# Optimization experiments

Measured on AMD Instinct MI355X. Metric: run time of the kernel, lower is better.

The kernel has to match this reference:

```python
import jax, jax.numpy as jnp
import numpy as np

OMEGA = 30.0
B = 65536
NUM_FREQ = 8  # int(base_dim / in_features) = 32 / 4


def _siren_w(k, out_dim, in_dim, first=False):
    bound = (1.0 / in_dim) if first else (np.sqrt(6.0 / in_dim) / OMEGA)
    return jax.random.uniform(k, (out_dim, in_dim), jnp.float32, -bound, bound)


def _lin_w(k, out_dim, in_dim):
    bound = np.sqrt(1.0 / in_dim)
    return jax.random.uniform(k, (out_dim, in_dim), jnp.float32, -bound, bound)


def setup_inputs() -> dict:
    key = jax.random.key(0)
    ks = jax.random.split(key, 16)
    E = 7
    d = {}
    d['x'] = jax.random.uniform(ks[0], (B, 4), jnp.float32, -1.0, 1.0)
    # encoder: pos_dim=64 -> sine1(128) -> sine2(256) -> resblock(256, bottleneck 128)
    d['enc_s1_w'] = _siren_w(ks[1], 128, 64, first=True); d['enc_s1_b'] = jnp.zeros((128,), jnp.float32)
    d['enc_s2_w'] = _siren_w(ks[2], 256, 128); d['enc_s2_b'] = jnp.zeros((256,), jnp.float32)
    d['res_fc1_w'] = _lin_w(ks[3], 128, 256); d['res_fc1_b'] = jnp.zeros((128,), jnp.float32)
    d['res_fc2_w'] = _lin_w(ks[4], 128, 128); d['res_fc2_b'] = jnp.zeros((128,), jnp.float32)
    d['res_fc3_w'] = _lin_w(ks[5], 256, 128); d['res_fc3_b'] = jnp.zeros((256,), jnp.float32)
    # policy: 4 -> 128 (first sine) -> 128 (sine); gate in = 256+128=384 -> 7
    d['pol_s1_w'] = _siren_w(ks[6], 128, 4, first=True); d['pol_s1_b'] = jnp.zeros((128,), jnp.float32)
    d['pol_s2_w'] = _siren_w(ks[7], 128, 128); d['pol_s2_b'] = jnp.zeros((128,), jnp.float32)
    d['gate_w'] = _siren_w(ks[8], 7, 384); d['gate_b'] = jnp.zeros((7,), jnp.float32)
    # 7 experts: SirenMLP 256 -> 256 (first sine) -> 256 (sine) -> final Linear 256 -> 1
    bnd1 = 1.0 / 256.0
    d['exp_s1_w'] = jax.random.uniform(ks[9], (E, 256, 256), jnp.float32, -bnd1, bnd1)
    d['exp_s1_b'] = jnp.zeros((E, 256), jnp.float32)
    bnd2 = np.sqrt(6.0 / 256.0) / OMEGA
    d['exp_s2_w'] = jax.random.uniform(ks[10], (E, 256, 256), jnp.float32, -bnd2, bnd2)
    d['exp_s2_b'] = jnp.zeros((E, 256), jnp.float32)
    d['exp_fin_w'] = jax.random.uniform(ks[11], (E, 1, 256), jnp.float32, -bnd2, bnd2)
    d['exp_fin_b'] = jnp.zeros((E, 1), jnp.float32)
    return d


def reference(x, enc_s1_w, enc_s1_b, enc_s2_w, enc_s2_b, res_fc1_w, res_fc1_b,
              res_fc2_w, res_fc2_b, res_fc3_w, res_fc3_b, pol_s1_w, pol_s1_b,
              pol_s2_w, pol_s2_b, gate_w, gate_b, exp_s1_w, exp_s1_b,
              exp_s2_w, exp_s2_b, exp_fin_w, exp_fin_b):
    # NeRF-style positional encoding: log-sampled freqs, no include_input
    freqs = (2.0 ** jnp.arange(NUM_FREQ, dtype=jnp.float32)) * jnp.pi  # [F]
    ang = x[:, :, None] * freqs                                        # [B,4,F]
    pe = jnp.concatenate([jnp.sin(ang), jnp.cos(ang)], axis=-1)        # [B,4,2F]
    pe = pe.reshape(x.shape[0], -1)                                    # [B,64]
    # shared encoder: sine1 -> sine2 -> bottleneck res block
    h = jnp.sin(OMEGA * (pe @ enc_s1_w.T + enc_s1_b))                  # [B,128]
    h = jnp.sin(OMEGA * (h @ enc_s2_w.T + enc_s2_b))                   # [B,256]
    r = jax.nn.relu(h @ res_fc1_w.T + res_fc1_b)                       # [B,128]
    r = jax.nn.relu(r @ res_fc2_w.T + res_fc2_b)                       # [B,128]
    r = r @ res_fc3_w.T + res_fc3_b                                    # [B,256]
    enc_feat = jax.nn.relu(r + h)                                      # [B,256]
    # policy: sine feature net + gate over [enc_feat, pol_feat]
    pf = jnp.sin(OMEGA * (x @ pol_s1_w.T + pol_s1_b))                  # [B,128]
    pf = jnp.sin(OMEGA * (pf @ pol_s2_w.T + pol_s2_b))                 # [B,128]
    logits = jnp.concatenate([enc_feat, pf], axis=-1) @ gate_w.T + gate_b  # [B,7]
    probs = jax.nn.softmax(logits, axis=-1)                            # [B,7]
    # all 7 expert SIREN MLPs as batched GEMMs over expert axis e
    e = jnp.sin(OMEGA * (jnp.einsum('bd,eod->beo', enc_feat, exp_s1_w) + exp_s1_b))  # [B,7,256]
    e = jnp.sin(OMEGA * (jnp.einsum('beh,eoh->beo', e, exp_s2_w) + exp_s2_b))        # [B,7,256]
    preds = jnp.einsum('beh,eoh->beo', e, exp_fin_w) + exp_fin_b                     # [B,7,1]
    # soft routing: probability-weighted combination
    y = jnp.sum(preds * probs[:, :, None], axis=1)                     # [B,1]
    return y
```

## Files before the change

### kernel.cpp

```cpp
#include <hip/hip_runtime.h>


typedef short v8s __attribute__((ext_vector_type(8)));
typedef float v4f __attribute__((ext_vector_type(4)));

#define KSIN 4.774648293f
#define AST 264
#define PST 9
#define N_CVT 8

__device__ __forceinline__ float bf2f(unsigned short h) {
  union { unsigned u; float f; } v; v.u = ((unsigned)h) << 16; return v.f;
}
__device__ __forceinline__ unsigned short f2bf(float f) {
  union { float f; unsigned u; } v; v.f = f;
  unsigned r = v.u + 0x7fffu + ((v.u >> 16) & 1u);
  return (unsigned short)(r >> 16);
}
__device__ __forceinline__ unsigned pack2(float a, float b) {
  return (unsigned)f2bf(a) | ((unsigned)f2bf(b) << 16);
}
__device__ __forceinline__ float sin_rev(float x) {
  return __builtin_amdgcn_sinf(x);
}
__device__ __forceinline__ float cos_rev(float x) {
  return __builtin_amdgcn_cosf(x);
}

struct CvtArgs {
  const float* src[N_CVT];
  unsigned     off[N_CVT];
  unsigned     n[N_CVT];
  float        scl[N_CVT];
};

__global__ void convert_kernel(CvtArgs a, unsigned short* __restrict__ dst) {
  const int tid = blockIdx.x * blockDim.x + threadIdx.x;
  const int stride = gridDim.x * blockDim.x;
  for (int k = 0; k < N_CVT; k++) {
    const unsigned n4 = a.n[k] >> 2;
    const float4* s = (const float4*)a.src[k];
    const float sc = a.scl[k];
    uint2* d = (uint2*)(dst + a.off[k]);
    for (unsigned i = tid; i < n4; i += stride) {
      float4 v = s[i];
      uint2 o; o.x = pack2(v.x * sc, v.y * sc); o.y = pack2(v.z * sc, v.w * sc);
      d[i] = o;
    }
    for (unsigned i = (n4 << 2) + tid; i < a.n[k]; i += stride)
      dst[a.off[k] + i] = f2bf(a.src[k][i] * sc);
  }
}

template<int K, int NPW, int ACT>
__device__ __forceinline__ void wgemm2(const unsigned short* A0,
                                       const unsigned short* A1,
                                       unsigned short* O0, unsigned short* O1,
                                       int oc,
                                       const unsigned short* __restrict__ W,
                                       const float* __restrict__ bias,
                                       const unsigned short* skip0,
                                       const unsigned short* skip1) {
  const int lane = threadIdx.x & 63;
  const int wave = threadIdx.x >> 6;
  const int m15  = lane & 15;
  const int q    = lane >> 4;
  const int n0   = wave * (NPW * 16);
  v4f acc[2][NPW][4];
#pragma unroll
  for (int tl = 0; tl < 2; tl++)
#pragma unroll
    for (int i = 0; i < NPW; i++)
#pragma unroll
      for (int j = 0; j < 4; j++) acc[tl][i][j] = (v4f){0.f, 0.f, 0.f, 0.f};

#pragma unroll
  for (int k0 = 0; k0 < K / 32; ++k0) {
    v8s b[NPW], a0[4], a1[4];
#pragma unroll
    for (int ct = 0; ct < NPW; ct++)
      b[ct] = *(const v8s*)(W + (size_t)(n0 + ct * 16 + m15) * K + k0 * 32 + q * 8);
#pragma unroll
    for (int rt = 0; rt < 4; rt++) {
      a0[rt] = *(const v8s*)(A0 + (rt * 16 + m15) * AST + k0 * 32 + q * 8);
      a1[rt] = *(const v8s*)(A1 + (rt * 16 + m15) * AST + k0 * 32 + q * 8);
    }
#pragma unroll
    for (int ct = 0; ct < NPW; ct++)
#pragma unroll
      for (int rt = 0; rt < 4; rt++) {
        acc[0][ct][rt] = __builtin_amdgcn_mfma_f32_16x16x32_bf16(b[ct], a0[rt], acc[0][ct][rt], 0, 0, 0);
        acc[1][ct][rt] = __builtin_amdgcn_mfma_f32_16x16x32_bf16(b[ct], a1[rt], acc[1][ct][rt], 0, 0, 0);
      }
  }

#pragma unroll
  for (int ct = 0; ct < NPW; ct++) {
    const int c0 = n0 + ct * 16 + q * 4;
    v4f bv = *(const v4f*)(bias + c0);
    if (ACT == 0) bv *= KSIN;
#pragma unroll
    for (int rt = 0; rt < 4; rt++) {
      const int row = rt * 16 + m15;
#pragma unroll
      for (int tl = 0; tl < 2; tl++) {
        const v4f av = acc[tl][ct][rt];
        unsigned short* OUT = tl ? O1 : O0;
        const unsigned short* skip = tl ? skip1 : skip0;
        float o0, o1, o2, o3;
        if (ACT == 2) {
          const uint2 sk = *(const uint2*)(skip + row * AST + c0);
          o0 = fmaxf(av[0] + bv[0] + bf2f((unsigned short)(sk.x & 0xffffu)), 0.f);
          o1 = fmaxf(av[1] + bv[1] + bf2f((unsigned short)(sk.x >> 16)), 0.f);
          o2 = fmaxf(av[2] + bv[2] + bf2f((unsigned short)(sk.y & 0xffffu)), 0.f);
          o3 = fmaxf(av[3] + bv[3] + bf2f((unsigned short)(sk.y >> 16)), 0.f);
        } else if (ACT == 1) {
          o0 = fmaxf(av[0] + bv[0], 0.f);
          o1 = fmaxf(av[1] + bv[1], 0.f);
          o2 = fmaxf(av[2] + bv[2], 0.f);
          o3 = fmaxf(av[3] + bv[3], 0.f);
        } else {
          o0 = sin_rev(av[0] + bv[0]);
          o1 = sin_rev(av[1] + bv[1]);
          o2 = sin_rev(av[2] + bv[2]);
          o3 = sin_rev(av[3] + bv[3]);
        }
        uint2 w2; w2.x = pack2(o0, o1); w2.y = pack2(o2, o3);
        *(uint2*)(OUT + row * AST + oc + c0) = w2;
      }
    }
  }
}

__device__ __forceinline__ void wgemm2q(const unsigned short* A0,
                                        const unsigned short* A1,
                                        unsigned short* O0, unsigned short* O1,
                                        const v8s (&qh)[2][2][4],
                                        const unsigned short* __restrict__ W,
                                        const float* __restrict__ bias) {
  const int lane = threadIdx.x & 63;
  const int wave = threadIdx.x >> 6;
  const int m15  = lane & 15;
  const int q    = lane >> 4;
  const int n0   = wave * 32;
  v4f acc[2][2][4];
#pragma unroll
  for (int tl = 0; tl < 2; tl++)
#pragma unroll
    for (int i = 0; i < 2; i++)
#pragma unroll
      for (int j = 0; j < 4; j++) acc[tl][i][j] = (v4f){0.f, 0.f, 0.f, 0.f};

#pragma unroll
  for (int k0 = 0; k0 < 8; ++k0) {
    v8s b[2], a0[4], a1[4];
#pragma unroll
    for (int ct = 0; ct < 2; ct++)
      b[ct] = *(const v8s*)(W + (size_t)(n0 + ct * 16 + m15) * 256 + k0 * 32 + q * 8);
#pragma unroll
    for (int rt = 0; rt < 4; rt++) {
      if (k0 < 2) {
        a0[rt] = qh[0][k0][rt];
        a1[rt] = qh[1][k0][rt];
      } else {
        a0[rt] = *(const v8s*)(A0 + (rt * 16 + m15) * AST + k0 * 32 + q * 8);
        a1[rt] = *(const v8s*)(A1 + (rt * 16 + m15) * AST + k0 * 32 + q * 8);
      }
    }
#pragma unroll
    for (int ct = 0; ct < 2; ct++)
#pragma unroll
      for (int rt = 0; rt < 4; rt++) {
        acc[0][ct][rt] = __builtin_amdgcn_mfma_f32_16x16x32_bf16(b[ct], a0[rt], acc[0][ct][rt], 0, 0, 0);
        acc[1][ct][rt] = __builtin_amdgcn_mfma_f32_16x16x32_bf16(b[ct], a1[rt], acc[1][ct][rt], 0, 0, 0);
      }
  }

#pragma unroll
  for (int ct = 0; ct < 2; ct++) {
    const int c0 = n0 + ct * 16 + q * 4;
    v4f bv = *(const v4f*)(bias + c0);
    bv *= KSIN;
#pragma unroll
    for (int rt = 0; rt < 4; rt++) {
      const int row = rt * 16 + m15;
#pragma unroll
      for (int tl = 0; tl < 2; tl++) {
        const v4f av = acc[tl][ct][rt];
        unsigned short* OUT = tl ? O1 : O0;
        float o0 = sin_rev(av[0] + bv[0]);
        float o1 = sin_rev(av[1] + bv[1]);
        float o2 = sin_rev(av[2] + bv[2]);
        float o3 = sin_rev(av[3] + bv[3]);
        uint2 w2; w2.x = pack2(o0, o1); w2.y = pack2(o2, o3);
        *(uint2*)(OUT + row * AST + c0) = w2;
      }
    }
  }
}

__device__ __forceinline__ void wexpert2d(const unsigned short* A0,
                                          const unsigned short* A1,
                                          const unsigned short* __restrict__ W,
                                          const float* __restrict__ bias,
                                          const float* __restrict__ wfin,
                                          float* __restrict__ pp0,
                                          float* __restrict__ pp1) {
  const int lane = threadIdx.x & 63;
  const int wave = threadIdx.x >> 6;
  const int m15  = lane & 15;
  const int q    = lane >> 4;
  const int n0   = wave * 32;
  v4f acc[2][2][4];
#pragma unroll
  for (int tl = 0; tl < 2; tl++)
#pragma unroll
    for (int i = 0; i < 2; i++)
#pragma unroll
      for (int j = 0; j < 4; j++) acc[tl][i][j] = (v4f){0.f, 0.f, 0.f, 0.f};

#pragma unroll
  for (int k0 = 0; k0 < 8; ++k0) {
    v8s b[2], a0[4], a1[4];
#pragma unroll
    for (int ct = 0; ct < 2; ct++)
      b[ct] = *(const v8s*)(W + (size_t)(n0 + ct * 16 + m15) * 256 + k0 * 32 + q * 8);
#pragma unroll
    for (int rt = 0; rt < 4; rt++) {
      a0[rt] = *(const v8s*)(A0 + (rt * 16 + m15) * AST + k0 * 32 + q * 8);
      a1[rt] = *(const v8s*)(A1 + (rt * 16 + m15) * AST + k0 * 32 + q * 8);
    }
#pragma unroll
    for (int ct = 0; ct < 2; ct++)
#pragma unroll
      for (int rt = 0; rt < 4; rt++) {
        acc[0][ct][rt] = __builtin_amdgcn_mfma_f32_16x16x32_bf16(b[ct], a0[rt], acc[0][ct][rt], 0, 0, 0);
        acc[1][ct][rt] = __builtin_amdgcn_mfma_f32_16x16x32_bf16(b[ct], a1[rt], acc[1][ct][rt], 0, 0, 0);
      }
  }

  float p0[4] = {0.f, 0.f, 0.f, 0.f};
  float p1[4] = {0.f, 0.f, 0.f, 0.f};
#pragma unroll
  for (int ct = 0; ct < 2; ct++) {
    const int c0 = n0 + ct * 16 + q * 4;
    v4f bv = *(const v4f*)(bias + c0);
    bv *= KSIN;
    const v4f wf = *(const v4f*)(wfin + c0);
#pragma unroll
    for (int rt = 0; rt < 4; rt++)
#pragma unroll
      for (int r = 0; r < 4; r++) {
        p0[rt] += sin_rev(acc[0][ct][rt][r] + bv[r]) * wf[r];
        p1[rt] += sin_rev(acc[1][ct][rt][r] + bv[r]) * wf[r];
      }
  }
#pragma unroll
  for (int rt = 0; rt < 4; rt++) {
    float v0 = p0[rt], v1 = p1[rt];
    v0 += __shfl_xor(v0, 16);
    v0 += __shfl_xor(v0, 32);
    v1 += __shfl_xor(v1, 16);
    v1 += __shfl_xor(v1, 32);
    if (q == 0) {
      pp0[wave * 64 + rt * 16 + m15] = v0;
      pp1[wave * 64 + rt * 16 + m15] = v1;
    }
  }
}

__global__ __launch_bounds__(512, 2) void moe_inr_kernel(
    const float* __restrict__ x,
    const unsigned short* __restrict__ es1w, const float* __restrict__ es1b,
    const unsigned short* __restrict__ es2w, const float* __restrict__ es2b,
    const unsigned short* __restrict__ rf1w, const float* __restrict__ rf1b,
    const unsigned short* __restrict__ rf2w, const float* __restrict__ rf2b,
    const unsigned short* __restrict__ rf3w, const float* __restrict__ rf3b,
    const float* __restrict__ ps1w,          const float* __restrict__ ps1b,
    const unsigned short* __restrict__ ps2w, const float* __restrict__ ps2b,
    const float* __restrict__ gw,            const float* __restrict__ gb,
    const unsigned short* __restrict__ xs1w, const float* __restrict__ xs1b,
    const unsigned short* __restrict__ xs2w, const float* __restrict__ xs2b,
    const float* __restrict__ xfw,           const float* __restrict__ xfb,
    float* __restrict__ out) {
  __shared__ __align__(16) unsigned short P[2][64 * AST];
  __shared__ __align__(16) unsigned short Q[2][64 * AST];
  __shared__ float probs[2][64 * PST];
  __shared__ float pred_part[2][8 * 64];

  const int t   = threadIdx.x;
  const int r0g = blockIdx.x * 128;

#pragma unroll
  for (int tl = 0; tl < 2; ++tl) {
    const int row = t & 63, g = t >> 6, c = g & 3, jh = g >> 2;
    const float xv = x[(r0g + tl * 64 + row) * 4 + c];
    float sn[4], cs[4];
#pragma unroll
    for (int jj = 0; jj < 4; jj++) {
      const int j = jh * 4 + jj;
      const float rev = xv * (0.5f * (float)(1 << j));
      sn[jj] = sin_rev(rev);
      cs[jj] = cos_rev(rev);
    }
    uint2 ws; ws.x = pack2(sn[0], sn[1]); ws.y = pack2(sn[2], sn[3]);
    uint2 wc2; wc2.x = pack2(cs[0], cs[1]); wc2.y = pack2(cs[2], cs[3]);
    *(uint2*)(P[tl] + row * AST + c * 16 + jh * 4) = ws;
    *(uint2*)(P[tl] + row * AST + c * 16 + 8 + jh * 4) = wc2;
  }
  __syncthreads();
  wgemm2<64, 1, 0>(P[0], P[1], P[0], P[1], 64, es1w, es1b, nullptr, nullptr);
  __syncthreads();
  wgemm2<128, 2, 0>(P[0] + 64, P[1] + 64, Q[0], Q[1], 0, es2w, es2b, nullptr, nullptr);
  __syncthreads();
  wgemm2<256, 1, 1>(Q[0], Q[1], P[0], P[1], 0, rf1w, rf1b, nullptr, nullptr);
  __syncthreads();
  wgemm2<128, 1, 1>(P[0], P[1], P[0], P[1], 128, rf2w, rf2b, nullptr, nullptr);
  __syncthreads();
  wgemm2<128, 2, 2>(P[0] + 128, P[1] + 128, Q[0], Q[1], 0, rf3w, rf3b, Q[0], Q[1]);
  __syncthreads();
#pragma unroll
  for (int tl = 0; tl < 2; ++tl) {
    const int row = t & 63, g = t >> 6;
    const v4f xv = *(const v4f*)(x + (r0g + tl * 64 + row) * 4);
#pragma unroll
    for (int ii = 0; ii < 4; ii++) {
      float oo[4];
#pragma unroll
      for (int i2 = 0; i2 < 4; i2++) {
        const int o = g * 16 + ii * 4 + i2;
        const v4f w4 = *(const v4f*)(ps1w + o * 4);
        const float z = xv[0] * w4[0] + xv[1] * w4[1] + xv[2] * w4[2] +
                        xv[3] * w4[3] + ps1b[o];
        oo[i2] = sin_rev(KSIN * z);
      }
      uint2 w2; w2.x = pack2(oo[0], oo[1]); w2.y = pack2(oo[2], oo[3]);
      *(uint2*)(P[tl] + row * AST + g * 16 + ii * 4) = w2;
    }
  }
  __syncthreads();
  wgemm2<128, 1, 0>(P[0], P[1], P[0], P[1], 128, ps2w, ps2b, nullptr, nullptr);
  __syncthreads();
#pragma unroll
  for (int tl = 0; tl < 2; ++tl) {
    const int row = t >> 3, pp = t & 7;
    float lg[7] = {0.f, 0.f, 0.f, 0.f, 0.f, 0.f, 0.f};
#pragma unroll
    for (int u = 0; u < 6; u++) {
      const int kk = pp * 48 + u * 8;
      const v8s av = (kk < 256) ? *(const v8s*)(Q[tl] + row * AST + kk)
                                : *(const v8s*)(P[tl] + row * AST + 128 + (kk - 256));
      float af[8];
#pragma unroll
      for (int e2 = 0; e2 < 8; e2++) af[e2] = bf2f((unsigned short)av[e2]);
#pragma unroll
      for (int j = 0; j < 7; j++) {
        const v4f g0 = *(const v4f*)(gw + j * 384 + kk);
        const v4f g1 = *(const v4f*)(gw + j * 384 + kk + 4);
        lg[j] += af[0] * g0[0] + af[1] * g0[1] + af[2] * g0[2] + af[3] * g0[3] +
                 af[4] * g1[0] + af[5] * g1[1] + af[6] * g1[2] + af[7] * g1[3];
      }
    }
#pragma unroll
    for (int j = 0; j < 7; j++) {
      float s = lg[j];
      s += __shfl_xor(s, 1);
      s += __shfl_xor(s, 2);
      s += __shfl_xor(s, 4);
      lg[j] = s;
    }
    if (pp == 0) {
#pragma unroll
      for (int j = 0; j < 7; j++) probs[tl][row * PST + j] = lg[j] + gb[j];
    }
  }
  __syncthreads();
  float yr = 0.f;
  if (t < 128) {
    const int tl = t >> 6, row = t & 63;
    float m = probs[tl][row * PST];
#pragma unroll
    for (int j = 1; j < 7; j++) m = fmaxf(m, probs[tl][row * PST + j]);
    float s = 0.f, e[7];
#pragma unroll
    for (int j = 0; j < 7; j++) { e[j] = __expf(probs[tl][row * PST + j] - m); s += e[j]; }
    const float inv = 1.f / s;
#pragma unroll
    for (int j = 0; j < 7; j++) probs[tl][row * PST + j] = e[j] * inv;
  }
  v8s qh[2][2][4];
  {
    const int m15 = t & 15, q = (t & 63) >> 4;
#pragma unroll
    for (int k0 = 0; k0 < 2; k0++)
#pragma unroll
      for (int rt = 0; rt < 4; rt++) {
        qh[0][k0][rt] = *(const v8s*)(Q[0] + (rt * 16 + m15) * AST + k0 * 32 + q * 8);
        qh[1][k0][rt] = *(const v8s*)(Q[1] + (rt * 16 + m15) * AST + k0 * 32 + q * 8);
      }
  }
  for (int ex = 0; ex < 7; ++ex) {
    wgemm2q(Q[0], Q[1], P[0], P[1], qh,
            xs1w + ex * 65536, xs1b + ex * 256);
    __syncthreads();
    wexpert2d(P[0], P[1], xs2w + ex * 65536, xs2b + ex * 256, xfw + ex * 256,
              pred_part[0], pred_part[1]);
    __syncthreads();
    if (t < 128) {
      const int tl = t >> 6, row = t & 63;
      float pr = 0.f;
#pragma unroll
      for (int w = 0; w < 8; w++) pr += pred_part[tl][w * 64 + row];
      yr += (pr + xfb[ex]) * probs[tl][row * PST + ex];
    }
  }
  if (t < 128) out[r0g + t] = yr;
}

extern "C" void kernel_launch(void* const* d_in, const int* in_sizes, int n_in,
                              void* d_out, int out_size, void* d_ws, size_t ws_size,
                              hipStream_t stream) {
  (void)out_size; (void)n_in; (void)ws_size;
  const int   idx[N_CVT] = {1, 3, 5, 7, 9, 13, 17, 19};
  const float scl[N_CVT] = {KSIN, KSIN, 1.f, 1.f, 1.f, KSIN, KSIN, KSIN};
  unsigned off[N_CVT], cur = 0;
  CvtArgs a;
  for (int i = 0; i < N_CVT; i++) {
    off[i] = cur;
    a.src[i] = (const float*)d_in[idx[i]];
    a.off[i] = cur;
    a.n[i]   = (unsigned)in_sizes[idx[i]];
    a.scl[i] = scl[i];
    cur += ((unsigned)in_sizes[idx[i]] + 7u) & ~7u;
  }
  unsigned short* dst = (unsigned short*)d_ws;
  hipLaunchKernelGGL(convert_kernel, dim3(1024), dim3(256), 0, stream, a, dst);
  hipLaunchKernelGGL(moe_inr_kernel, dim3(65536 / 128), dim3(512), 0, stream,
      (const float*)d_in[0],
      dst + off[0], (const float*)d_in[2],
      dst + off[1], (const float*)d_in[4],
      dst + off[2], (const float*)d_in[6],
      dst + off[3], (const float*)d_in[8],
      dst + off[4], (const float*)d_in[10],
      (const float*)d_in[11], (const float*)d_in[12],
      dst + off[5], (const float*)d_in[14],
      (const float*)d_in[15], (const float*)d_in[16],
      dst + off[6], (const float*)d_in[18],
      dst + off[7], (const float*)d_in[20],
      (const float*)d_in[21], (const float*)d_in[22],
      (float*)d_out);
}
```

Measured before the change: 329.8 us.

## Software-pipeline next expert's first-layer GEMM with current expert's second layer

Splits the expert first-layer GEMM into an MFMA accumulation phase and a sine/store epilogue. The next expert's layer-1 accumulation is issued right after the current expert's layer-2 work, before the barrier, so MFMA work can overlap barrier waits and the softmax. The epilogue then writes P after the barrier, with an extra barrier per iteration. The change also drops the register cache of the first Q k-slices, and the accumulators stay live across the layer-2 call, which raises register pressure and risks lower occupancy or spills.

```diff
diff --git a/kernel.cpp b/kernel.cpp
--- a/kernel.cpp
+++ b/kernel.cpp
@@ -132,18 +132,15 @@
   }
 }
 
-__device__ __forceinline__ void wgemm2q(const unsigned short* A0,
+__device__ __forceinline__ void e1_mfma(const unsigned short* A0,
                                         const unsigned short* A1,
-                                        unsigned short* O0, unsigned short* O1,
-                                        const v8s (&qh)[2][2][4],
                                         const unsigned short* __restrict__ W,
-                                        const float* __restrict__ bias) {
+                                        v4f (&acc)[2][2][4]) {
   const int lane = threadIdx.x & 63;
   const int wave = threadIdx.x >> 6;
   const int m15  = lane & 15;
   const int q    = lane >> 4;
   const int n0   = wave * 32;
-  v4f acc[2][2][4];
 #pragma unroll
   for (int tl = 0; tl < 2; tl++)
 #pragma unroll
@@ -159,13 +156,8 @@
       b[ct] = *(const v8s*)(W + (size_t)(n0 + ct * 16 + m15) * 256 + k0 * 32 + q * 8);
 #pragma unroll
     for (int rt = 0; rt < 4; rt++) {
-      if (k0 < 2) {
-        a0[rt] = qh[0][k0][rt];
-        a1[rt] = qh[1][k0][rt];
-      } else {
-        a0[rt] = *(const v8s*)(A0 + (rt * 16 + m15) * AST + k0 * 32 + q * 8);
-        a1[rt] = *(const v8s*)(A1 + (rt * 16 + m15) * AST + k0 * 32 + q * 8);
-      }
+      a0[rt] = *(const v8s*)(A0 + (rt * 16 + m15) * AST + k0 * 32 + q * 8);
+      a1[rt] = *(const v8s*)(A1 + (rt * 16 + m15) * AST + k0 * 32 + q * 8);
     }
 #pragma unroll
     for (int ct = 0; ct < 2; ct++)
@@ -175,7 +167,16 @@
         acc[1][ct][rt] = __builtin_amdgcn_mfma_f32_16x16x32_bf16(b[ct], a1[rt], acc[1][ct][rt], 0, 0, 0);
       }
   }
-
+}
+
+__device__ __forceinline__ void e1_epi(const v4f (&acc)[2][2][4],
+                                       const float* __restrict__ bias,
+                                       unsigned short* O0, unsigned short* O1) {
+  const int lane = threadIdx.x & 63;
+  const int wave = threadIdx.x >> 6;
+  const int m15  = lane & 15;
+  const int q    = lane >> 4;
+  const int n0   = wave * 32;
 #pragma unroll
   for (int ct = 0; ct < 2; ct++) {
     const int c0 = n0 + ct * 16 + q * 4;
@@ -376,6 +377,8 @@
   }
   __syncthreads();
   float yr = 0.f;
+  v4f acc1[2][2][4];
+  e1_mfma(Q[0], Q[1], xs1w, acc1);
   if (t < 128) {
     const int tl = t >> 6, row = t & 63;
     float m = probs[tl][row * PST];
@@ -388,24 +391,14 @@
 #pragma unroll
     for (int j = 0; j < 7; j++) probs[tl][row * PST + j] = e[j] * inv;
   }
-  v8s qh[2][2][4];
-  {
-    const int m15 = t & 15, q = (t & 63) >> 4;
-#pragma unroll
-    for (int k0 = 0; k0 < 2; k0++)
-#pragma unroll
-      for (int rt = 0; rt < 4; rt++) {
-        qh[0][k0][rt] = *(const v8s*)(Q[0] + (rt * 16 + m15) * AST + k0 * 32 + q * 8);
-        qh[1][k0][rt] = *(const v8s*)(Q[1] + (rt * 16 + m15) * AST + k0 * 32 + q * 8);
-      }
-  }
+  e1_epi(acc1, xs1b, P[0], P[1]);
+  __syncthreads();
   for (int ex = 0; ex < 7; ++ex) {
-    wgemm2q(Q[0], Q[1], P[0], P[1], qh,
-            xs1w + ex * 65536, xs1b + ex * 256);
-    __syncthreads();
     wexpert2d(P[0], P[1], xs2w + ex * 65536, xs2b + ex * 256, xfw + ex * 256,
               pred_part[0], pred_part[1]);
+    if (ex < 6) e1_mfma(Q[0], Q[1], xs1w + (ex + 1) * 65536, acc1);
     __syncthreads();
+    if (ex < 6) e1_epi(acc1, xs1b + (ex + 1) * 256, P[0], P[1]);
     if (t < 128) {
       const int tl = t >> 6, row = t & 63;
       float pr = 0.f;
@@ -413,6 +406,7 @@
       for (int w = 0; w < 8; w++) pr += pred_part[tl][w * 64 + row];
       yr += (pr + xfb[ex]) * probs[tl][row * PST + ex];
     }
+    if (ex < 6) __syncthreads();
   }
   if (t < 128) out[r0g + t] = yr;
 }
```

After: 320.9 us. 2.7% less time.
